# Kernel optimization log

Hardware: AMD Instinct MI355X
Metric: run time of the kernel (lower is better)

Reference implementation:

```python
import jax, jax.numpy as jnp
import numpy as np

N = 50000      # nodes
E = 800000     # edges (avg degree 16)
D = 128        # d_model
C = 2          # num_classes
F_IN = 8       # GCNConv(8, d_model)


def setup_inputs() -> dict:
    key = jax.random.key(0)
    ks = jax.random.split(key, 12)
    s = 0.05  # weight init scale
    return {
        "feature_vec": jax.random.normal(ks[0], (N, F_IN), dtype=jnp.float32),
        "bboxes": jax.random.uniform(ks[1], (N, 4), dtype=jnp.float32),
        "bbox_indices": jnp.arange(N, dtype=jnp.int64) if jax.config.jax_enable_x64 else jnp.arange(N, dtype=jnp.int32),
        "edge_index": jax.random.randint(ks[2], (2, E), 0, N, dtype=jnp.int32),
        "W1": jax.random.normal(ks[3], (F_IN, D), dtype=jnp.float32) * s,
        "b1": jnp.zeros((D,), dtype=jnp.float32),
        "W2": jax.random.normal(ks[4], (D, D), dtype=jnp.float32) * s,
        "b2": jnp.zeros((D,), dtype=jnp.float32),
        "lin1_W": jax.random.normal(ks[5], (2 * D, D), dtype=jnp.float32) * s,
        "lin1_b": jnp.zeros((D,), dtype=jnp.float32),
        "linf_W": jax.random.normal(ks[6], (D, C), dtype=jnp.float32) * s,
        "linf_b": jnp.zeros((C,), dtype=jnp.float32),
    }


def gcn_conv(x, W, b, edge_index, n):
    """PyG GCNConv: add self-loops, symmetric D^-1/2 A D^-1/2 normalization."""
    x = x @ W                                   # [n, out]
    sl = jnp.arange(n, dtype=edge_index.dtype)
    row = jnp.concatenate([edge_index[0], sl])  # source
    col = jnp.concatenate([edge_index[1], sl])  # target
    ones = jnp.ones(row.shape[0], dtype=x.dtype)
    deg = jax.ops.segment_sum(ones, col, num_segments=n)  # >= 1 due to self-loops
    dinv = jax.lax.rsqrt(deg)
    norm = dinv[row] * dinv[col]                # [E + n]
    msg = x[row] * norm[:, None]                # gather + scale
    out = jax.ops.segment_sum(msg, col, num_segments=n)   # scatter-aggregate
    return out + b


def reference(feature_vec, bboxes, bbox_indices, edge_index,
              W1, b1, W2, b2, lin1_W, lin1_b, linf_W, linf_b):
    n = feature_vec.shape[0]
    x = jax.nn.relu(gcn_conv(feature_vec, W1, b1, edge_index, n))
    x = jax.nn.relu(gcn_conv(x, W2, b2, edge_index, n))
    x1 = x[edge_index[0]]                        # [E, D]
    x2 = x[edge_index[1]]                        # [E, D]
    xpair = jnp.concatenate([x1, x2], axis=-1)   # [E, 2D]
    xpair = jax.nn.relu(xpair @ lin1_W + lin1_b)
    xfin = xpair @ linf_W + linf_b               # [E, C]
    probs = jax.nn.log_softmax(xfin, axis=-1)
    bbox_pairs = jnp.concatenate([bboxes[edge_index[0]], bboxes[edge_index[1]]], axis=-1)  # [E, 8]
    bbox_index_pairs = jnp.stack([bbox_indices[edge_index[0]], bbox_indices[edge_index[1]]], axis=1)  # [E, 2]
    return (probs, bbox_pairs, bbox_index_pairs)
```

## Files before the change

### kernel.cpp

```cpp
#include <hip/hip_runtime.h>
#include <hip/hip_bf16.h>
#include <math.h>


typedef __attribute__((ext_vector_type(8))) short short8;
typedef __attribute__((ext_vector_type(4))) float f32x4;
typedef __attribute__((ext_vector_type(2))) float fv2;

__device__ inline ushort f2bf(float f) {
    union { __hip_bfloat16 h; ushort u; } cv;
    cv.h = __float2bfloat16(f);
    return cv.u;
}
__device__ inline float bf2f(ushort u) {
    union { float f; uint u; } c;
    c.u = ((uint)u) << 16;
    return c.f;
}
__device__ inline uchar f2fp8(float f) {
    uint p = __builtin_amdgcn_cvt_pk_fp8_f32(f, f, 0u, false);
    return (uchar)(p & 0xffu);
}

__global__ void k_hist(const int* __restrict__ col, int* __restrict__ cnt, int E) {
    int e = blockIdx.x * blockDim.x + threadIdx.x;
    if (e < E) atomicAdd(&cnt[col[e]], 1);
}

__global__ __launch_bounds__(1024) void k_bsum(const int* __restrict__ cnt,
                                               int* __restrict__ bsum, int N) {
    __shared__ int ts[1024];
    const int b = blockIdx.x, t = threadIdx.x;
    const int i0 = b * 2048 + 2 * t;
    int a0 = (i0 < N) ? cnt[i0] : 0;
    int a1 = (i0 + 1 < N) ? cnt[i0 + 1] : 0;
    ts[t] = a0 + a1;
    __syncthreads();
#pragma unroll
    for (int off = 512; off > 0; off >>= 1) {
        if (t < off) ts[t] += ts[t + off];
        __syncthreads();
    }
    if (t == 0) bsum[b] = ts[0];
}

__global__ __launch_bounds__(1024) void k_scanw(const int* __restrict__ cnt,
                                                const int* __restrict__ bsum,
                                                int* __restrict__ ptr, int N, int E) {
    __shared__ int ts[1024];
    const int b = blockIdx.x, t = threadIdx.x;
    int boff = 0;
    for (int i = 0; i < b; ++i) boff += bsum[i];
    const int i0 = b * 2048 + 2 * t;
    const int a0 = (i0 < N) ? cnt[i0] : 0;
    const int a1 = (i0 + 1 < N) ? cnt[i0 + 1] : 0;
    const int s = a0 + a1;
    ts[t] = s;
    __syncthreads();
    for (int off = 1; off < 1024; off <<= 1) {
        int v = (t >= off) ? ts[t - off] : 0;
        __syncthreads();
        ts[t] += v;
        __syncthreads();
    }
    const int excl = boff + ts[t] - s;
    if (i0 < N) ptr[i0] = excl;
    if (i0 + 1 < N) ptr[i0 + 1] = excl + a0;
    if (b == 0 && t == 0) ptr[N] = E;
}

__global__ void k_fill(const int* __restrict__ row, const int* __restrict__ col,
                       const int* __restrict__ cnt, const int* __restrict__ ptr,
                       int* __restrict__ cursor, int2* __restrict__ eadj, int E) {
    int e = blockIdx.x * blockDim.x + threadIdx.x;
    if (e >= E) return;
    int r = row[e], c = col[e];
    float dr = rsqrtf(1.0f + (float)cnt[r]);
    float dc = rsqrtf(1.0f + (float)cnt[c]);
    int p = ptr[c] + atomicAdd(&cursor[c], 1);
    eadj[p] = make_int2(r, __float_as_int(dr * dc));
}

__global__ void k_prepW(const float* __restrict__ lin1W, const float* __restrict__ W2,
                        ushort* __restrict__ Wuv, ushort* __restrict__ W2t) {
    int tid = blockIdx.x * blockDim.x + threadIdx.x;
    if (tid < 256 * 128) {
        int c = tid >> 7, k = tid & 127;
        int krow = k + ((c >> 7) << 7);
        Wuv[tid] = f2bf(lin1W[krow * 128 + (c & 127)]);
    } else if (tid < 256 * 128 + 128 * 128) {
        int u = tid - 256 * 128;
        int n = u >> 7, k = u & 127;
        W2t[u] = f2bf(W2[k * 128 + n]);
    }
}

__global__ __launch_bounds__(256) void k_l1(const float* __restrict__ feat,
                                            const int* __restrict__ cnt,
                                            const int* __restrict__ ptr,
                                            const int2* __restrict__ eadj,
                                            const float* __restrict__ W1,
                                            const float* __restrict__ b1,
                                            ushort* __restrict__ x1, int N) {
    __shared__ float sagg[32][8];
    __shared__ float sW1[8 * 128];
    const int tid = threadIdx.x;
    for (int i = tid; i < 1024; i += 256) sW1[i] = W1[i];

    const int lane8 = tid & 7;
    const int nloc = tid >> 3;
    const int node = blockIdx.x * 32 + nloc;
    float acc = 0.f;
    if (node < N) {
        float dd = 1.0f / (1.0f + (float)cnt[node]);
        acc = feat[(size_t)node * 8 + lane8] * dd;
        int i = ptr[node], end = ptr[node + 1];
        for (; i < end; ++i) {
            const int2 a = eadj[i];
            acc += feat[(size_t)a.x * 8 + lane8] * __int_as_float(a.y);
        }
    }
    sagg[nloc][lane8] = acc;
    __syncthreads();

    if (node < N) {
        const int jb = lane8 * 16;
        float av[8];
#pragma unroll
        for (int k = 0; k < 8; ++k) av[k] = sagg[nloc][k];
        short8 r0, r1;
#pragma unroll
        for (int j = 0; j < 16; ++j) {
            float s = b1[jb + j];
#pragma unroll
            for (int k = 0; k < 8; ++k) s = fmaf(av[k], sW1[k * 128 + jb + j], s);
            const ushort bv = f2bf(fmaxf(s, 0.f));
            if (j < 8) r0[j] = (short)bv; else r1[j - 8] = (short)bv;
        }
        *reinterpret_cast<short8*>(&x1[(size_t)node * 128 + jb]) = r0;
        *reinterpret_cast<short8*>(&x1[(size_t)node * 128 + jb + 8]) = r1;
    }
}

__global__ __launch_bounds__(256) void k_gemm2(const ushort* __restrict__ x1,
                                               const ushort* __restrict__ W2t,
                                               uchar* __restrict__ h2, int N) {
    __shared__ ushort ldsW[128 * 128];
    const int tid = threadIdx.x;
    const int wave = tid >> 6, lane = tid & 63;
    const int m = lane & 15, kb = lane >> 4;
    const int n0 = blockIdx.x * 64;

    const int node_a = min(n0 + wave * 16 + m, N - 1);
    short8 a[4];
#pragma unroll
    for (int kk = 0; kk < 4; ++kk) {
        a[kk] = *reinterpret_cast<const short8*>(&x1[(size_t)node_a * 128 + kk * 32 + kb * 8]);
    }

    {
        char* lb = reinterpret_cast<char*>(ldsW);
        const short8* wg = reinterpret_cast<const short8*>(W2t);
#pragma unroll
        for (int i = 0; i < 8; ++i) {
            const int g = i * 256 + tid;
            const int bo = g * 16;
            const int swz = bo ^ (((bo >> 8) & 7) << 4);
            *reinterpret_cast<short8*>(lb + swz) = wg[g];
        }
    }
    __syncthreads();

    f32x4 acc[8];
#pragma unroll
    for (int t = 0; t < 8; ++t) acc[t] = (f32x4){0.f, 0.f, 0.f, 0.f};

    const char* lbr = reinterpret_cast<const char*>(ldsW);
    const int mswz = (m & 7) << 4;
#pragma unroll
    for (int kk = 0; kk < 4; ++kk) {
#pragma unroll
        for (int t = 0; t < 8; ++t) {
            const int bo = (t * 16 + m) * 256 + kk * 64 + kb * 16;
            const short8 b = *reinterpret_cast<const short8*>(lbr + (bo ^ mswz));
            acc[t] = __builtin_amdgcn_mfma_f32_16x16x32_bf16(a[kk], b, acc[t], 0, 0, 0);
        }
    }

#pragma unroll
    for (int r = 0; r < 4; ++r) {
        const int node = n0 + wave * 16 + kb * 4 + r;
        if (node < N) {
#pragma unroll
            for (int t = 0; t < 8; ++t) {
                h2[(size_t)node * 128 + t * 16 + m] = f2fp8(acc[t][r]);
            }
        }
    }
}

__global__ __launch_bounds__(256) void k_gather2(const uchar* __restrict__ h2,
                                                 const int* __restrict__ cnt,
                                                 const int* __restrict__ ptr,
                                                 const int2* __restrict__ eadj,
                                                 const float* __restrict__ b2,
                                                 ushort* __restrict__ xbf, int N) {
    const int lane8 = threadIdx.x & 7;
    const int node = blockIdx.x * 32 + (threadIdx.x >> 3);
    if (node >= N) return;
    const float dd = 1.0f / (1.0f + (float)cnt[node]);
    float acc[16];
    {
        const uint4 w = *reinterpret_cast<const uint4*>(&h2[(size_t)node * 128 + lane8 * 16]);
        const uint ws[4] = {w.x, w.y, w.z, w.w};
#pragma unroll
        for (int q = 0; q < 4; ++q) {
            const fv2 lo = __builtin_amdgcn_cvt_pk_f32_fp8(ws[q], false);
            const fv2 hi = __builtin_amdgcn_cvt_pk_f32_fp8(ws[q], true);
            acc[4 * q + 0] = lo[0] * dd;
            acc[4 * q + 1] = lo[1] * dd;
            acc[4 * q + 2] = hi[0] * dd;
            acc[4 * q + 3] = hi[1] * dd;
        }
    }
    int i = ptr[node];
    const int end = ptr[node + 1];
    for (; i < end; ++i) {
        const int2 aa = eadj[i];
        const float nm = __int_as_float(aa.y);
        const uint4 w = *reinterpret_cast<const uint4*>(&h2[(size_t)aa.x * 128 + lane8 * 16]);
        const uint ws[4] = {w.x, w.y, w.z, w.w};
#pragma unroll
        for (int q = 0; q < 4; ++q) {
            const fv2 lo = __builtin_amdgcn_cvt_pk_f32_fp8(ws[q], false);
            const fv2 hi = __builtin_amdgcn_cvt_pk_f32_fp8(ws[q], true);
            acc[4 * q + 0] = fmaf(lo[0], nm, acc[4 * q + 0]);
            acc[4 * q + 1] = fmaf(lo[1], nm, acc[4 * q + 1]);
            acc[4 * q + 2] = fmaf(hi[0], nm, acc[4 * q + 2]);
            acc[4 * q + 3] = fmaf(hi[1], nm, acc[4 * q + 3]);
        }
    }
    short8 r0, r1;
#pragma unroll
    for (int q = 0; q < 8; ++q) {
        r0[q] = (short)f2bf(fmaxf(acc[q] + b2[lane8 * 16 + q], 0.f));
        r1[q] = (short)f2bf(fmaxf(acc[8 + q] + b2[lane8 * 16 + 8 + q], 0.f));
    }
    *reinterpret_cast<short8*>(&xbf[(size_t)node * 128 + lane8 * 16]) = r0;
    *reinterpret_cast<short8*>(&xbf[(size_t)node * 128 + lane8 * 16 + 8]) = r1;
}

__global__ __launch_bounds__(512) void k_gemm_uv(const ushort* __restrict__ xbf,
                                                 const ushort* __restrict__ Wuv,
                                                 const float* __restrict__ lin1b,
                                                 uchar* __restrict__ uv, int N) {
    __shared__ ushort ldsW[256 * 128];
    const int tid = threadIdx.x;
    const int wave = tid >> 6, lane = tid & 63;
    const int m = lane & 15, kb = lane >> 4;
    const int ng = wave >> 1;
    const int ch = wave & 1;
    const int n0 = blockIdx.x * 64 + ng * 16;

    const int node_a = min(n0 + m, N - 1);
    short8 a[4];
#pragma unroll
    for (int kk = 0; kk < 4; ++kk) {
        a[kk] = *reinterpret_cast<const short8*>(&xbf[(size_t)node_a * 128 + kk * 32 + kb * 8]);
    }

    {
        char* lb = reinterpret_cast<char*>(ldsW);
        const short8* wg = reinterpret_cast<const short8*>(Wuv);
#pragma unroll
        for (int i = 0; i < 8; ++i) {
            const int g = i * 512 + tid;
            const int bo = g * 16;
            const int swz = bo ^ (((bo >> 8) & 7) << 4);
            *reinterpret_cast<short8*>(lb + swz) = wg[g];
        }
    }
    __syncthreads();

    f32x4 acc[8];
#pragma unroll
    for (int t = 0; t < 8; ++t) acc[t] = (f32x4){0.f, 0.f, 0.f, 0.f};

    const char* lbr = reinterpret_cast<const char*>(ldsW);
    const int mswz = (m & 7) << 4;
#pragma unroll
    for (int kk = 0; kk < 4; ++kk) {
#pragma unroll
        for (int t = 0; t < 8; ++t) {
            const int bo = (ch * 128 + t * 16 + m) * 256 + kk * 64 + kb * 16;
            const short8 b = *reinterpret_cast<const short8*>(lbr + (bo ^ mswz));
            acc[t] = __builtin_amdgcn_mfma_f32_16x16x32_bf16(a[kk], b, acc[t], 0, 0, 0);
        }
    }

#pragma unroll
    for (int r = 0; r < 4; ++r) {
        const int node = n0 + kb * 4 + r;
        if (node < N) {
#pragma unroll
            for (int t = 0; t < 8; ++t) {
                const int c = t * 16 + m;
                float av = acc[t][r];
                if (ch == 0) av += lin1b[c];
                uv[(size_t)node * 256 + ch * 128 + c] = f2fp8(av);
            }
        }
    }
}

__global__ __launch_bounds__(256) void k_edge_lite(const uchar* __restrict__ uv,
                                                   const float* __restrict__ linfW,
                                                   const float* __restrict__ linfb,
                                                   const float* __restrict__ bboxes,
                                                   const int* __restrict__ bidx,
                                                   const int* __restrict__ row,
                                                   const int* __restrict__ col,
                                                   float* __restrict__ out_probs,
                                                   float* __restrict__ out_bbox,
                                                   float* __restrict__ out_bidx,
                                                   int E) {
    const int lane8 = threadIdx.x & 7;
    const int slot = threadIdx.x >> 3;
    int e = blockIdx.x * 32 + slot;
    if (e >= E) return;

    float wd[16];
#pragma unroll
    for (int j = 0; j < 16; ++j) {
        const int c = lane8 * 16 + j;
        wd[j] = linfW[c * 2] - linfW[c * 2 + 1];
    }
    const float bias_d = linfb[0] - linfb[1];
    const int step = gridDim.x * 32;

    int s = row[e], d = col[e];
    uint4 ua = *reinterpret_cast<const uint4*>(&uv[(size_t)s * 256 + lane8 * 16]);
    uint4 va = *reinterpret_cast<const uint4*>(&uv[(size_t)d * 256 + 128 + lane8 * 16]);

    while (true) {
        const int e2 = e + step;
        const bool more = (e2 < E);
        int s2 = 0, d2 = 0;
        uint4 ua2 = ua, va2 = va;
        if (more) {
            s2 = row[e2];
            d2 = col[e2];
            ua2 = *reinterpret_cast<const uint4*>(&uv[(size_t)s2 * 256 + lane8 * 16]);
            va2 = *reinterpret_cast<const uint4*>(&uv[(size_t)d2 * 256 + 128 + lane8 * 16]);
        }

        float p = 0.f;
        {
            const uint uw[4] = {ua.x, ua.y, ua.z, ua.w};
            const uint vw[4] = {va.x, va.y, va.z, va.w};
#pragma unroll
            for (int w = 0; w < 4; ++w) {
                const fv2 ul = __builtin_amdgcn_cvt_pk_f32_fp8(uw[w], false);
                const fv2 uh = __builtin_amdgcn_cvt_pk_f32_fp8(uw[w], true);
                const fv2 vl = __builtin_amdgcn_cvt_pk_f32_fp8(vw[w], false);
                const fv2 vh = __builtin_amdgcn_cvt_pk_f32_fp8(vw[w], true);
                p = fmaf(fmaxf(ul[0] + vl[0], 0.f), wd[4 * w + 0], p);
                p = fmaf(fmaxf(ul[1] + vl[1], 0.f), wd[4 * w + 1], p);
                p = fmaf(fmaxf(uh[0] + vh[0], 0.f), wd[4 * w + 2], p);
                p = fmaf(fmaxf(uh[1] + vh[1], 0.f), wd[4 * w + 3], p);
            }
        }
        p += __shfl_xor(p, 1);
        p += __shfl_xor(p, 2);
        p += __shfl_xor(p, 4);

        out_bbox[(size_t)e * 8 + lane8] = bboxes[(size_t)((lane8 < 4) ? s : d) * 4 + (lane8 & 3)];
        if (lane8 == 0) {
            *reinterpret_cast<float2*>(&out_bidx[(size_t)e * 2]) =
                make_float2((float)bidx[s], (float)bidx[d]);
        } else if (lane8 == 1) {
            const float dd = p + bias_d;
            const float ad = fabsf(dd);
            const float t = -log1pf(expf(-ad));
            const float2 pr = (dd >= 0.f) ? make_float2(t, t - ad) : make_float2(t - ad, t);
            *reinterpret_cast<float2*>(&out_probs[(size_t)e * 2]) = pr;
        }

        if (!more) break;
        e = e2; s = s2; d = d2; ua = ua2; va = va2;
    }
}

extern "C" void kernel_launch(void* const* d_in, const int* in_sizes, int n_in,
                              void* d_out, int out_size, void* d_ws, size_t ws_size,
                              hipStream_t stream) {
    const float* feat   = (const float*)d_in[0];
    const float* bboxes = (const float*)d_in[1];
    const int*   bidx   = (const int*)d_in[2];
    const int*   eidx   = (const int*)d_in[3];
    const float* W1     = (const float*)d_in[4];
    const float* b1     = (const float*)d_in[5];
    const float* W2     = (const float*)d_in[6];
    const float* b2     = (const float*)d_in[7];
    const float* lin1W  = (const float*)d_in[8];
    const float* lin1b  = (const float*)d_in[9];
    const float* linfW  = (const float*)d_in[10];
    const float* linfb  = (const float*)d_in[11];

    const int N = in_sizes[0] / 8;
    const int E = in_sizes[3] / 2;
    const int* row = eidx;
    const int* col = eidx + E;

    size_t Np = ((size_t)N + 255) & ~255ull;
    size_t Ep = ((size_t)E + 255) & ~255ull;
    int*    cnt    = (int*)d_ws;
    int*    cursor = cnt + Np;
    int*    ptr    = cursor + Np;
    int*    bsum   = ptr + Np + 256;
    int2*   eadj   = (int2*)(bsum + 256);
    ushort* x1     = (ushort*)(eadj + Ep);
    uchar*  h2     = (uchar*)(x1 + (size_t)N * 128);
    uchar*  uvbuf  = h2 + (size_t)N * 128;
    ushort* Wuv    = (ushort*)(uvbuf + (size_t)N * 256);
    ushort* W2t    = Wuv + 256 * 128;
    ushort* xbf    = x1;

    float* out       = (float*)d_out;
    float* out_probs = out;
    float* out_bbox  = out + (size_t)E * 2;
    float* out_bidx  = out + (size_t)E * 10;

    const int B = 256;
    const int nchunk = (N + 2047) / 2048;

    hipMemsetAsync(cnt, 0, 2 * Np * sizeof(int), stream);
    k_hist<<<(E + B - 1) / B, B, 0, stream>>>(col, cnt, E);
    k_bsum<<<nchunk, 1024, 0, stream>>>(cnt, bsum, N);
    k_scanw<<<nchunk, 1024, 0, stream>>>(cnt, bsum, ptr, N, E);
    k_fill<<<(E + B - 1) / B, B, 0, stream>>>(row, col, cnt, ptr, cursor, eadj, E);
    k_prepW<<<(256 * 128 + 128 * 128 + B - 1) / B, B, 0, stream>>>(lin1W, W2, Wuv, W2t);

    k_l1<<<(N + 31) / 32, B, 0, stream>>>(feat, cnt, ptr, eadj, W1, b1, x1, N);

    k_gemm2<<<(N + 63) / 64, B, 0, stream>>>(x1, W2t, h2, N);
    k_gather2<<<(N + 31) / 32, B, 0, stream>>>(h2, cnt, ptr, eadj, b2, xbf, N);

    k_gemm_uv<<<(N + 63) / 64, 512, 0, stream>>>(xbf, Wuv, lin1b, uvbuf, N);

    k_edge_lite<<<2048, B, 0, stream>>>(uvbuf, linfW, linfb,
                                        bboxes, bidx, row, col,
                                        out_probs, out_bbox, out_bidx, E);
}
```

Before: 219.1 us.

## Process edge classifier per destination node via CSR to reuse destination row

The final edge kernel now walks the CSR built earlier, grouped by destination node. Each 8-lane group loads and decodes the destination's v-half, bbox and index once, then reuses them for all incoming edges. This removes one random 128-byte gather per edge. In exchange, k_fill must store the original edge id, outputs are written in scattered order rather than sequentially, and load balance now follows node in-degree.

```diff
diff --git a/kernel.cpp b/kernel.cpp
--- a/kernel.cpp
+++ b/kernel.cpp
@@ -71,7 +71,8 @@
 
 __global__ void k_fill(const int* __restrict__ row, const int* __restrict__ col,
                        const int* __restrict__ cnt, const int* __restrict__ ptr,
-                       int* __restrict__ cursor, int2* __restrict__ eadj, int E) {
+                       int* __restrict__ cursor, int2* __restrict__ eadj,
+                       int* __restrict__ eorig, int E) {
     int e = blockIdx.x * blockDim.x + threadIdx.x;
     if (e >= E) return;
     int r = row[e], c = col[e];
@@ -79,6 +80,7 @@
     float dc = rsqrtf(1.0f + (float)cnt[c]);
     int p = ptr[c] + atomicAdd(&cursor[c], 1);
     eadj[p] = make_int2(r, __float_as_int(dr * dc));
+    eorig[p] = e;
 }
 
 __global__ void k_prepW(const float* __restrict__ lin1W, const float* __restrict__ W2,
@@ -313,71 +315,88 @@
     }
 }
 
-__global__ __launch_bounds__(256) void k_edge_lite(const uchar* __restrict__ uv,
-                                                   const float* __restrict__ linfW,
-                                                   const float* __restrict__ linfb,
-                                                   const float* __restrict__ bboxes,
-                                                   const int* __restrict__ bidx,
-                                                   const int* __restrict__ row,
-                                                   const int* __restrict__ col,
-                                                   float* __restrict__ out_probs,
-                                                   float* __restrict__ out_bbox,
-                                                   float* __restrict__ out_bidx,
-                                                   int E) {
+__global__ __launch_bounds__(256) void k_edge_csr(const uchar* __restrict__ uv,
+                                                  const int* __restrict__ ptr,
+                                                  const int2* __restrict__ eadj,
+                                                  const int* __restrict__ eorig,
+                                                  const float* __restrict__ linfW,
+                                                  const float* __restrict__ linfb,
+                                                  const float* __restrict__ bboxes,
+                                                  const int* __restrict__ bidx,
+                                                  float* __restrict__ out_probs,
+                                                  float* __restrict__ out_bbox,
+                                                  float* __restrict__ out_bidx,
+                                                  int N) {
     const int lane8 = threadIdx.x & 7;
-    const int slot = threadIdx.x >> 3;
-    int e = blockIdx.x * 32 + slot;
-    if (e >= E) return;
+    const int c = blockIdx.x * 32 + (threadIdx.x >> 3);
+    if (c >= N) return;
 
     float wd[16];
 #pragma unroll
     for (int j = 0; j < 16; ++j) {
-        const int c = lane8 * 16 + j;
-        wd[j] = linfW[c * 2] - linfW[c * 2 + 1];
+        const int ch = lane8 * 16 + j;
+        wd[j] = linfW[ch * 2] - linfW[ch * 2 + 1];
     }
     const float bias_d = linfb[0] - linfb[1];
-    const int step = gridDim.x * 32;
-
-    int s = row[e], d = col[e];
+
+    float vch[16];
+    {
+        const uint4 va = *reinterpret_cast<const uint4*>(&uv[(size_t)c * 256 + 128 + lane8 * 16]);
+        const uint ws[4] = {va.x, va.y, va.z, va.w};
+#pragma unroll
+        for (int q = 0; q < 4; ++q) {
+            const fv2 lo = __builtin_amdgcn_cvt_pk_f32_fp8(ws[q], false);
+            const fv2 hi = __builtin_amdgcn_cvt_pk_f32_fp8(ws[q], true);
+            vch[4 * q + 0] = lo[0];
+            vch[4 * q + 1] = lo[1];
+            vch[4 * q + 2] = hi[0];
+            vch[4 * q + 3] = hi[1];
+        }
+    }
+    const float bb_dst = bboxes[(size_t)c * 4 + (lane8 & 3)];
+    const float fid_dst = (float)bidx[c];
+
+    int i = ptr[c];
+    const int end = ptr[c + 1];
+    if (i >= end) return;
+
+    int s = eadj[i].x;
+    int e = eorig[i];
     uint4 ua = *reinterpret_cast<const uint4*>(&uv[(size_t)s * 256 + lane8 * 16]);
-    uint4 va = *reinterpret_cast<const uint4*>(&uv[(size_t)d * 256 + 128 + lane8 * 16]);
 
     while (true) {
-        const int e2 = e + step;
-        const bool more = (e2 < E);
-        int s2 = 0, d2 = 0;
-        uint4 ua2 = ua, va2 = va;
+        const int inext = i + 1;
+        const bool more = (inext < end);
+        int s2 = 0, e2 = 0;
+        uint4 ua2 = ua;
         if (more) {
-            s2 = row[e2];
-            d2 = col[e2];
+            s2 = eadj[inext].x;
+            e2 = eorig[inext];
             ua2 = *reinterpret_cast<const uint4*>(&uv[(size_t)s2 * 256 + lane8 * 16]);
-            va2 = *reinterpret_cast<const uint4*>(&uv[(size_t)d2 * 256 + 128 + lane8 * 16]);
         }
 
         float p = 0.f;
         {
             const uint uw[4] = {ua.x, ua.y, ua.z, ua.w};
-            const uint vw[4] = {va.x, va.y, va.z, va.w};
-#pragma unroll
-            for (int w = 0; w < 4; ++w) {
-                const fv2 ul = __builtin_amdgcn_cvt_pk_f32_fp8(uw[w], false);
-                const fv2 uh = __builtin_amdgcn_cvt_pk_f32_fp8(uw[w], true);
-                const fv2 vl = __builtin_amdgcn_cvt_pk_f32_fp8(vw[w], false);
-                const fv2 vh = __builtin_amdgcn_cvt_pk_f32_fp8(vw[w], true);
-                p = fmaf(fmaxf(ul[0] + vl[0], 0.f), wd[4 * w + 0], p);
-                p = fmaf(fmaxf(ul[1] + vl[1], 0.f), wd[4 * w + 1], p);
-                p = fmaf(fmaxf(uh[0] + vh[0], 0.f), wd[4 * w + 2], p);
-                p = fmaf(fmaxf(uh[1] + vh[1], 0.f), wd[4 * w + 3], p);
+#pragma unroll
+            for (int q = 0; q < 4; ++q) {
+                const fv2 ul = __builtin_amdgcn_cvt_pk_f32_fp8(uw[q], false);
+                const fv2 uh = __builtin_amdgcn_cvt_pk_f32_fp8(uw[q], true);
+                p = fmaf(fmaxf(ul[0] + vch[4 * q + 0], 0.f), wd[4 * q + 0], p);
+                p = fmaf(fmaxf(ul[1] + vch[4 * q + 1], 0.f), wd[4 * q + 1], p);
+                p = fmaf(fmaxf(uh[0] + vch[4 * q + 2], 0.f), wd[4 * q + 2], p);
+                p = fmaf(fmaxf(uh[1] + vch[4 * q + 3], 0.f), wd[4 * q + 3], p);
             }
         }
         p += __shfl_xor(p, 1);
         p += __shfl_xor(p, 2);
         p += __shfl_xor(p, 4);
 
-        out_bbox[(size_t)e * 8 + lane8] = bboxes[(size_t)((lane8 < 4) ? s : d) * 4 + (lane8 & 3)];
+        out_bbox[(size_t)e * 8 + lane8] =
+            (lane8 < 4) ? bboxes[(size_t)s * 4 + lane8] : bb_dst;
         if (lane8 == 0) {
             *reinterpret_cast<float2*>(&out_bidx[(size_t)e * 2]) =
-                make_float2((float)bidx[s], (float)bidx[d]);
+                make_float2((float)bidx[s], fid_dst);
         } else if (lane8 == 1) {
             const float dd = p + bias_d;
             const float ad = fabsf(dd);
@@ -387,7 +406,7 @@
         }
 
         if (!more) break;
-        e = e2; s = s2; d = d2; ua = ua2; va = va2;
+        i = inext; s = s2; e = e2; ua = ua2;
     }
 }
 
@@ -419,7 +438,8 @@
     int*    ptr    = cursor + Np;
     int*    bsum   = ptr + Np + 256;
     int2*   eadj   = (int2*)(bsum + 256);
-    ushort* x1     = (ushort*)(eadj + Ep);
+    int*    eorig  = (int*)(eadj + Ep);
+    ushort* x1     = (ushort*)(eorig + Ep);
     uchar*  h2     = (uchar*)(x1 + (size_t)N * 128);
     uchar*  uvbuf  = h2 + (size_t)N * 128;
     ushort* Wuv    = (ushort*)(uvbuf + (size_t)N * 256);
@@ -438,7 +458,7 @@
     k_hist<<<(E + B - 1) / B, B, 0, stream>>>(col, cnt, E);
     k_bsum<<<nchunk, 1024, 0, stream>>>(cnt, bsum, N);
     k_scanw<<<nchunk, 1024, 0, stream>>>(cnt, bsum, ptr, N, E);
-    k_fill<<<(E + B - 1) / B, B, 0, stream>>>(row, col, cnt, ptr, cursor, eadj, E);
+    k_fill<<<(E + B - 1) / B, B, 0, stream>>>(row, col, cnt, ptr, cursor, eadj, eorig, E);
     k_prepW<<<(256 * 128 + 128 * 128 + B - 1) / B, B, 0, stream>>>(lin1W, W2, Wuv, W2t);
 
     k_l1<<<(N + 31) / 32, B, 0, stream>>>(feat, cnt, ptr, eadj, W1, b1, x1, N);
@@ -448,7 +468,7 @@
 
     k_gemm_uv<<<(N + 63) / 64, 512, 0, stream>>>(xbf, Wuv, lin1b, uvbuf, N);
 
-    k_edge_lite<<<2048, B, 0, stream>>>(uvbuf, linfW, linfb,
-                                        bboxes, bidx, row, col,
-                                        out_probs, out_bbox, out_bidx, E);
-}
+    k_edge_csr<<<(N + 31) / 32, B, 0, stream>>>(uvbuf, ptr, eadj, eorig,
+                                                linfW, linfb, bboxes, bidx,
+                                                out_probs, out_bbox, out_bidx, N);
+}
```

New measurement: 279.5 us. 27.5% more time.
